# Kernel optimization log

Measured on AMD Instinct MI355X. Metric: run time of the kernel, lower is better.

The kernel has to match this reference:

```python
import jax, jax.numpy as jnp
import numpy as np

EMB = 768
HEADS = 12
HEAD_DIM = EMB // HEADS
FF = 4 * EMB
EPS = 1e-5


def setup_inputs() -> dict:
    key = jax.random.key(0)
    ks = jax.random.split(key, 12)
    s = 0.02
    return {
        "x": jax.random.normal(ks[0], (4, 2048, EMB), dtype=jnp.float32),
        "ln1_scale": jnp.ones((EMB,), jnp.float32),
        "ln1_shift": jnp.zeros((EMB,), jnp.float32),
        # weights stored [in, out] (transpose of torch Linear layout)
        "wq": jax.random.normal(ks[1], (EMB, EMB), jnp.float32) * s,
        "wk": jax.random.normal(ks[2], (EMB, EMB), jnp.float32) * s,
        "wv": jax.random.normal(ks[3], (EMB, EMB), jnp.float32) * s,
        "wo": jax.random.normal(ks[4], (EMB, EMB), jnp.float32) * s,
        "bo": jnp.zeros((EMB,), jnp.float32),
        "ln2_scale": jnp.ones((EMB,), jnp.float32),
        "ln2_shift": jnp.zeros((EMB,), jnp.float32),
        "w1": jax.random.normal(ks[5], (EMB, FF), jnp.float32) * s,
        "b1": jnp.zeros((FF,), jnp.float32),
        "w2": jax.random.normal(ks[6], (FF, EMB), jnp.float32) * s,
        "b2": jnp.zeros((EMB,), jnp.float32),
    }


def _layernorm(x, scale, shift):
    mean = jnp.mean(x, axis=-1, keepdims=True)
    var = jnp.mean(jnp.square(x - mean), axis=-1, keepdims=True)  # unbiased=False
    return scale * (x - mean) / jnp.sqrt(var + EPS) + shift


def _gelu_tanh(x):
    c = jnp.sqrt(jnp.float32(2.0 / np.pi))
    return 0.5 * x * (1.0 + jnp.tanh(c * (x + 0.044715 * x * x * x)))


def _attention(x, wq, wk, wv, wo, bo):
    b, s, _ = x.shape
    q = (x @ wq).reshape(b, s, HEADS, HEAD_DIM).transpose(0, 2, 1, 3)
    k = (x @ wk).reshape(b, s, HEADS, HEAD_DIM).transpose(0, 2, 1, 3)
    v = (x @ wv).reshape(b, s, HEADS, HEAD_DIM).transpose(0, 2, 1, 3)
    scores = jnp.einsum("bhqd,bhkd->bhqk", q, k)  # [B,H,S,S]
    causal = jnp.tril(jnp.ones((s, s), dtype=bool))
    scores = jnp.where(causal, scores, -jnp.inf)
    weights = jax.nn.softmax(scores / jnp.sqrt(jnp.float32(HEAD_DIM)), axis=-1)
    ctx = jnp.einsum("bhqk,bhkd->bhqd", weights, v)
    ctx = ctx.transpose(0, 2, 1, 3).reshape(b, s, EMB)
    return ctx @ wo + bo


def reference(x, ln1_scale, ln1_shift, wq, wk, wv, wo, bo,
              ln2_scale, ln2_shift, w1, b1, w2, b2):
    # dropout rate is 0.0 (inference) -> identity
    x = x + _attention(_layernorm(x, ln1_scale, ln1_shift), wq, wk, wv, wo, bo)
    h = _layernorm(x, ln2_scale, ln2_shift)
    h = _gelu_tanh(h @ w1 + b1) @ w2 + b2
    return x + h
```

## Files before the change

### kernel.cpp

```cpp
#include <hip/hip_runtime.h>
#include <stdint.h>

#define EMB 768
#define SEQ 2048
#define BATCH 4
#define NHEADS 12
#define HDIM 64
#define FFDIM 3072
#define NTOK (BATCH*SEQ)
#define LNEPS 1e-5f
#define QSCALE 0.1803368801111137f

typedef __attribute__((ext_vector_type(8))) short bf16x8;
typedef __attribute__((ext_vector_type(4))) float f32x4;

__device__ __forceinline__ uint16_t f2bf(float f){
  union { float f; uint32_t u; } v; v.f = f;
  uint32_t r = v.u + 0x7fffu + ((v.u >> 16) & 1u);
  return (uint16_t)(r >> 16);
}
__device__ __forceinline__ uint32_t pk_rhu(float lo, float hi){
  union { float f; uint32_t u; } a, b; a.f = lo; b.f = hi;
  return __builtin_amdgcn_perm(b.u + 0x8000u, a.u + 0x8000u, 0x07060302u);
}

typedef __attribute__((address_space(3))) uint32_t lds32_t;
typedef __attribute__((address_space(1))) const uint32_t glb32_t;
__device__ __forceinline__ void gload16(const void* g, void* l){
  __builtin_amdgcn_global_load_lds((glb32_t*)(uintptr_t)g,
                                   (lds32_t*)(uintptr_t)l, 16, 0, 0);
}

struct TPtrs { const float* src[6]; uint16_t* dst[6]; };
__global__ __launch_bounds__(256) void transpose_all(TPtrs tp){
  int idx = blockIdx.x;
  int which, bx, by, K, N;
  if (idx < 2304){ which = idx/576; int l = idx - which*576; bx = l%24; by = l/24; K = 768;  N = 768;  }
  else if (idx < 4608){ which = 4; int l = idx-2304; bx = l%96; by = l/96; K = 768;  N = 3072; }
  else { which = 5; int l = idx-4608; bx = l%24; by = l/24; K = 3072; N = 768;  }
  const float* w = tp.src[which];
  uint16_t* wt   = tp.dst[which];
  __shared__ uint16_t tile[32][33];
  int n0 = bx*32, k0 = by*32;
  #pragma unroll
  for (int i=0;i<4;i++){
    int k = threadIdx.y + i*8;
    tile[k][threadIdx.x] = f2bf(w[(size_t)(k0+k)*N + n0 + threadIdx.x]);
  }
  __syncthreads();
  #pragma unroll
  for (int i=0;i<4;i++){
    int n = threadIdx.y + i*8;
    wt[(size_t)(n0+n)*K + k0 + threadIdx.x] = tile[threadIdx.x][n];
  }
}

__global__ __launch_bounds__(256) void ln_kernel(const float* __restrict__ x,
    const float* __restrict__ sc, const float* __restrict__ sh,
    uint16_t* __restrict__ out)
{
  int row = blockIdx.x*4 + (threadIdx.x>>6);
  int ln = threadIdx.x & 63;
  const float4* xr = (const float4*)(x + (size_t)row*EMB);
  float4 v0 = xr[ln], v1 = xr[64+ln], v2 = xr[128+ln];
  float s  = v0.x+v0.y+v0.z+v0.w + v1.x+v1.y+v1.z+v1.w + v2.x+v2.y+v2.z+v2.w;
  float s2 = v0.x*v0.x+v0.y*v0.y+v0.z*v0.z+v0.w*v0.w
           + v1.x*v1.x+v1.y*v1.y+v1.z*v1.z+v1.w*v1.w
           + v2.x*v2.x+v2.y*v2.y+v2.z*v2.z+v2.w*v2.w;
  #pragma unroll
  for (int off=1;off<64;off<<=1){ s += __shfl_xor(s,off); s2 += __shfl_xor(s2,off); }
  float mean = s*(1.f/768.f);
  float var  = s2*(1.f/768.f) - mean*mean;
  float rstd = rsqrtf(var + LNEPS);
  uint16_t* orow = out + (size_t)row*EMB;
  float4 vv[3] = {v0,v1,v2};
  #pragma unroll
  for (int i=0;i<3;i++){
    int c = (i*64+ln)*4;
    ushort4 o4;
    o4.x = f2bf((vv[i].x-mean)*rstd*sc[c+0] + sh[c+0]);
    o4.y = f2bf((vv[i].y-mean)*rstd*sc[c+1] + sh[c+1]);
    o4.z = f2bf((vv[i].z-mean)*rstd*sc[c+2] + sh[c+2]);
    o4.w = f2bf((vv[i].w-mean)*rstd*sc[c+3] + sh[c+3]);
    *(ushort4*)(orow + c) = o4;
  }
}

template<int MODE, int TM>
__global__ __launch_bounds__(256, 4) void gemm_bt(const uint16_t* __restrict__ A,
    const uint16_t* __restrict__ Bt0,
    const float* __restrict__ bias,
    const float* __restrict__ resid,
    void* __restrict__ outp,
    uint16_t* __restrict__ vt_out,
    int N, int K, long bt_zstride, long out_zstride)
{
  constexpr int MI = TM/32;
  __shared__ __align__(16) uint16_t As[2][TM][32];
  __shared__ __align__(16) uint16_t Bs[2][128][32];
  const uint16_t* Bt = Bt0 + (size_t)blockIdx.z * bt_zstride;
  int tid = threadIdx.x;
  int wave = tid>>6, ln = tid&63, lane16 = ln&15, quad = ln>>4;
  int m0 = blockIdx.x*TM, n0 = blockIdx.y*128;
  int wm = (wave>>1)*(MI*16), wn = (wave&1)*64;
  f32x4 zf = {0.f,0.f,0.f,0.f};
  f32x4 acc[MI][4];
  #pragma unroll
  for (int i=0;i<MI;i++)
    #pragma unroll
    for (int j=0;j<4;j++) acc[i][j]=zf;
  int ar = tid>>2;
  int ac = (tid&3)*8;
  const uint16_t* Arow0 = A  + (size_t)(m0+ar)*K    + ac;
  const uint16_t* Arow1 = A  + (size_t)(m0+ar+64)*K + ac;
  const uint16_t* Brow0 = Bt + (size_t)(n0+ar)*K    + ac;
  const uint16_t* Brow1 = Bt + (size_t)(n0+ar+64)*K + ac;

  auto stage = [&](int buf, int k0){
    char* lA = (char*)&As[buf][0][0] + wave*1024;
    char* lB = (char*)&Bs[buf][0][0] + wave*1024;
    gload16(Arow0 + k0, lA);
    if (TM==128) gload16(Arow1 + k0, lA + 4096);
    gload16(Brow0 + k0, lB);
    gload16(Brow1 + k0, lB + 4096);
  };

  int niter = K>>5;
  stage(0, 0);
  for (int s=0; s<niter; s++){
    __syncthreads();
    if (s+1 < niter) stage((s+1)&1, (s+1)<<5);
    int buf = s&1;
    bf16x8 af[MI], bfr[4];
    #pragma unroll
    for (int mi=0;mi<MI;mi++) af[mi]  = *(const bf16x8*)&As[buf][wm+mi*16+lane16][quad*8];
    #pragma unroll
    for (int ni=0;ni<4;ni++)  bfr[ni] = *(const bf16x8*)&Bs[buf][wn+ni*16+lane16][quad*8];
    #pragma unroll
    for (int mi=0;mi<MI;mi++)
      #pragma unroll
      for (int ni=0;ni<4;ni++)
        acc[mi][ni] = __builtin_amdgcn_mfma_f32_16x16x32_bf16(af[mi], bfr[ni], acc[mi][ni], 0,0,0);
  }
  if (MODE==0 && blockIdx.z==2){
    #pragma unroll
    for (int mi=0;mi<MI;mi++){
      int mrow0 = m0 + wm + mi*16 + quad*4;
      int bb = mrow0 >> 11, s = mrow0 & 2047;
      #pragma unroll
      for (int ni=0;ni<4;ni++){
        int ncol = n0 + wn + ni*16 + lane16;
        int hh = ncol >> 6, dd = ncol & 63;
        ushort4 o4 = { f2bf(acc[mi][ni][0]), f2bf(acc[mi][ni][1]),
                       f2bf(acc[mi][ni][2]), f2bf(acc[mi][ni][3]) };
        *(ushort4*)(vt_out + ((size_t)((bb*NHEADS+hh)*HDIM + dd))*SEQ + s) = o4;
      }
    }
    return;
  }
  float oscale = (MODE==0 && blockIdx.z==0) ? QSCALE : 1.0f;
  #pragma unroll
  for (int mi=0;mi<MI;mi++){
    #pragma unroll
    for (int r=0;r<4;r++){
      int mrow = m0 + wm + mi*16 + quad*4 + r;
      #pragma unroll
      for (int ni=0;ni<4;ni++){
        int ncol = n0 + wn + ni*16 + lane16;
        float vv = acc[mi][ni][r];
        size_t idx = (size_t)mrow*N + ncol;
        if (MODE==0){
          ((uint16_t*)outp)[(size_t)blockIdx.z*out_zstride + idx] = f2bf(vv*oscale);
        } else if (MODE==1){
          ((float*)outp)[idx] = vv + bias[ncol] + resid[idx];
        } else if (MODE==2){
          float t = vv + bias[ncol];
          float u = 1.5957691216057308f*(t + 0.044715f*t*t*t);
          ((uint16_t*)outp)[idx] = f2bf(t / (1.f + __expf(-u)));
        } else {
          ((float*)outp)[idx] = vv + bias[ncol] + resid[idx];
        }
      }
    }
  }
}

__global__ __launch_bounds__(256, 3) void attn_kernel(const uint16_t* __restrict__ q,
    const uint16_t* __restrict__ k, const uint16_t* __restrict__ vt,
    uint16_t* __restrict__ ctx)
{
  __shared__ __align__(16) uint16_t Ks[2][8][64][8];
  __shared__ __align__(16) uint16_t Vs[2][8][64][8];
  const f32x4 zf = {0.f,0.f,0.f,0.f};
  int tid = threadIdx.x;
  int wave = tid>>6, ln = tid&63, l16 = ln&15, quad = ln>>4;
  int id  = blockIdx.x;
  int xcd = id & 7;
  int s_  = id >> 3;
  int p   = s_ & 15;
  int g   = xcd*6 + (s_ >> 4);
  int h   = g % NHEADS, b = g / NHEADS;
  size_t kgbase = ((size_t)(b*SEQ + ln))*EMB + h*HDIM;
  size_t vgbase = ((size_t)((b*NHEADS + h)*HDIM + ln))*SEQ;

  f32x4 o[4];
  float m_l, l_l;
  bf16x8 qf0, qf1;
  int q0w, myq;

  auto stage = [&](int buf, int kv0){
    #pragma unroll
    for (int i=0;i<2;i++){
      int c = wave + 4*i;
      gload16(k  + kgbase + (size_t)kv0*EMB + c*8, &Ks[buf][c][0][0]);
      gload16(vt + vgbase + kv0 + c*8,             &Vs[buf][c][0][0]);
    }
  };
  auto init_tile = [&](int tile){
    q0w = tile*64 + wave*16;
    myq = q0w + l16;
    const uint16_t* qrow = q + ((size_t)(b*SEQ + q0w + l16))*EMB + h*HDIM + quad*8;
    qf0 = *(const bf16x8*)(qrow);
    qf1 = *(const bf16x8*)(qrow + 32);
    o[0]=zf; o[1]=zf; o[2]=zf; o[3]=zf;
    m_l = -3.0e38f; l_l = 0.f;
  };
  auto writeout = [&](){
    float inv = 1.0f / l_l;
    uint16_t* crow = ctx + ((size_t)(b*SEQ + q0w + l16))*EMB + h*HDIM + quad*4;
    #pragma unroll
    for (int t=0; t<4; t++){
      ushort4 w4 = { f2bf(o[t][0]*inv), f2bf(o[t][1]*inv),
                     f2bf(o[t][2]*inv), f2bf(o[t][3]*inv) };
      *(ushort4*)(crow + t*16) = w4;
    }
  };
  auto compute = [&](int buf, int kv0, bool masked){
    bf16x8 kf[4][2], vf[2][4];
    #pragma unroll
    for (int f=0; f<4; f++){
      kf[f][0] = *(const bf16x8*)&Ks[buf][quad  ][f*16+l16][0];
      kf[f][1] = *(const bf16x8*)&Ks[buf][quad+4][f*16+l16][0];
    }
    #pragma unroll
    for (int t=0; t<4; t++){
      vf[0][t] = *(const bf16x8*)&Vs[buf][quad  ][t*16+l16][0];
      vf[1][t] = *(const bf16x8*)&Vs[buf][quad+4][t*16+l16][0];
    }
    f32x4 st[4];
    #pragma unroll
    for (int f=0; f<4; f++){
      st[f] = __builtin_amdgcn_mfma_f32_16x16x32_bf16(kf[f][0], qf0, zf, 0,0,0);
      st[f] = __builtin_amdgcn_mfma_f32_16x16x32_bf16(kf[f][1], qf1, st[f], 0,0,0);
    }
    if (masked){
      #pragma unroll
      for (int f=0; f<4; f++){
        int kvf = kv0 + f*16 + quad*4;
        #pragma unroll
        for (int r=0; r<4; r++)
          if (kvf + r > myq) st[f][r] = -1e30f;
      }
    }
    float cmax = -1e30f;
    #pragma unroll
    for (int f=0; f<4; f++)
      #pragma unroll
      for (int r=0; r<4; r++) cmax = fmaxf(cmax, st[f][r]);
    cmax = fmaxf(cmax, __shfl_xor(cmax,16));
    cmax = fmaxf(cmax, __shfl_xor(cmax,32));
    float mn = fmaxf(m_l, cmax);
    float alpha = __builtin_amdgcn_exp2f(m_l - mn);
    float rs = 0.f;
    #pragma unroll
    for (int f=0; f<4; f++)
      #pragma unroll
      for (int r=0; r<4; r++){
        st[f][r] = __builtin_amdgcn_exp2f(st[f][r] - mn);
        rs += st[f][r];
      }
    rs += __shfl_xor(rs,16); rs += __shfl_xor(rs,32);
    l_l = l_l*alpha + rs; m_l = mn;
    #pragma unroll
    for (int t=0; t<4; t++)
      #pragma unroll
      for (int r=0; r<4; r++) o[t][r] *= alpha;
    uint32_t dw[4][2];
    #pragma unroll
    for (int f=0; f<4; f++){
      dw[f][0] = pk_rhu(st[f][0], st[f][1]);
      dw[f][1] = pk_rhu(st[f][2], st[f][3]);
    }
    union { uint32_t u[4]; bf16x8 v; } pb[2];
    #pragma unroll
    for (int g2=0; g2<2; g2++)
      #pragma unroll
      for (int j=0; j<4; j++){
        int src = 16*(2*(quad&1) + (j>>1)) + l16;
        uint32_t lo = (uint32_t)__shfl((int)dw[2*g2  ][j&1], src, 64);
        uint32_t hi = (uint32_t)__shfl((int)dw[2*g2+1][j&1], src, 64);
        pb[g2].u[j] = (quad>>1) ? hi : lo;
      }
    #pragma unroll
    for (int t=0; t<4; t++){
      o[t] = __builtin_amdgcn_mfma_f32_16x16x32_bf16(vf[0][t], pb[0].v, o[t], 0,0,0);
      o[t] = __builtin_amdgcn_mfma_f32_16x16x32_bf16(vf[1][t], pb[1].v, o[t], 0,0,0);
    }
  };

  int n0 = p + 1, ntot = 33;
  init_tile(p);
  stage(0, 0);
  for (int s=0; s<ntot; s++){
    int sl = (s < n0) ? s : s - n0;
    int kv0 = sl*64;
    __syncthreads();
    if (s+1 < ntot){
      int sn = s+1;
      int snl = (sn < n0) ? sn : sn - n0;
      stage(sn&1, snl*64);
    }
    if (s == n0){ writeout(); init_tile(31 - p); }
    bool masked = (s == n0-1) || (s == ntot-1);
    compute(s&1, kv0, masked);
  }
  writeout();
}

extern "C" void kernel_launch(void* const* d_in, const int* in_sizes, int n_in,
                              void* d_out, int out_size, void* d_ws, size_t ws_size,
                              hipStream_t stream) {
  const float* x     = (const float*)d_in[0];
  const float* ln1_s = (const float*)d_in[1];
  const float* ln1_b = (const float*)d_in[2];
  const float* wq    = (const float*)d_in[3];
  const float* wk    = (const float*)d_in[4];
  const float* wv    = (const float*)d_in[5];
  const float* wo    = (const float*)d_in[6];
  const float* bo    = (const float*)d_in[7];
  const float* ln2_s = (const float*)d_in[8];
  const float* ln2_b = (const float*)d_in[9];
  const float* w1    = (const float*)d_in[10];
  const float* b1    = (const float*)d_in[11];
  const float* w2    = (const float*)d_in[12];
  const float* b2    = (const float*)d_in[13];

  uint16_t* wqkv_t = (uint16_t*)d_ws;
  uint16_t* wo_t   = wqkv_t + 3*EMB*EMB;
  uint16_t* w1_t   = wo_t   + EMB*EMB;
  uint16_t* w2_t   = w1_t   + (size_t)FFDIM*EMB;
  uint16_t* xn     = w2_t   + (size_t)EMB*FFDIM;
  uint16_t* qkv    = xn     + (size_t)NTOK*EMB;
  uint16_t* ctx    = qkv    + (size_t)3*NTOK*EMB;
  uint16_t* hff    = qkv;
  float*    x1     = (float*)(ctx + (size_t)NTOK*EMB);
  uint16_t* vt     = (uint16_t*)(x1 + (size_t)NTOK*EMB);

  TPtrs tp;
  tp.src[0]=wq; tp.src[1]=wk; tp.src[2]=wv; tp.src[3]=wo; tp.src[4]=w1; tp.src[5]=w2;
  tp.dst[0]=wqkv_t; tp.dst[1]=wqkv_t+EMB*EMB; tp.dst[2]=wqkv_t+2*EMB*EMB;
  tp.dst[3]=wo_t; tp.dst[4]=w1_t; tp.dst[5]=w2_t;
  transpose_all<<<6912, dim3(32,8), 0, stream>>>(tp);

  ln_kernel<<<NTOK/4, 256, 0, stream>>>(x, ln1_s, ln1_b, xn);
  gemm_bt<0,128><<<dim3(NTOK/128, EMB/128, 3), 256, 0, stream>>>(
      xn, wqkv_t, nullptr, nullptr, qkv, vt, EMB, EMB,
      (long)EMB*EMB, (long)NTOK*EMB);
  attn_kernel<<<768, 256, 0, stream>>>(
      qkv, qkv + (size_t)NTOK*EMB, vt, ctx);
  gemm_bt<1,64><<<dim3(NTOK/64, EMB/128, 1), 256, 0, stream>>>(
      ctx, wo_t, bo, x, x1, nullptr, EMB, EMB, 0, 0);
  ln_kernel<<<NTOK/4, 256, 0, stream>>>(x1, ln2_s, ln2_b, xn);
  gemm_bt<2,128><<<dim3(NTOK/128, FFDIM/128, 1), 256, 0, stream>>>(
      xn, w1_t, b1, nullptr, hff, nullptr, FFDIM, EMB, 0, 0);
  gemm_bt<3,64><<<dim3(NTOK/64, EMB/128, 1), 256, 0, stream>>>(
      hff, w2_t, b2, x1, d_out, nullptr, EMB, FFDIM, 0, 0);
}
```

Measured before the change: 380.7 us.

## Rewrite attention with 32x32 MFMA, two waves per block, lazy rescaling

The attention kernel now uses two waves per 64-query tile, with 32 queries per wave, instead of four waves with 16 each. The QK^T and PV products move from 16x16x32 to 32x32x16 bf16 MFMA, which reduces LDS fragment reloads and cross-lane shuffles when building the P operand. It also uses the hardware v_cvt_pk_bf16_f32 conversion, raises wave priority around the MFMA sections, and skips the online-softmax rescale when the running max grows by 6 or less. Each block now has fewer waves, so hiding latency depends on having more blocks resident. The skipped rescale relies on fp32 headroom to tolerate the stale max.

```diff
diff --git a/kernel.cpp b/kernel.cpp
--- a/kernel.cpp
+++ b/kernel.cpp
@@ -13,15 +13,17 @@
 
 typedef __attribute__((ext_vector_type(8))) short bf16x8;
 typedef __attribute__((ext_vector_type(4))) float f32x4;
+typedef __attribute__((ext_vector_type(16))) float f32x16;
 
 __device__ __forceinline__ uint16_t f2bf(float f){
   union { float f; uint32_t u; } v; v.f = f;
   uint32_t r = v.u + 0x7fffu + ((v.u >> 16) & 1u);
   return (uint16_t)(r >> 16);
 }
-__device__ __forceinline__ uint32_t pk_rhu(float lo, float hi){
-  union { float f; uint32_t u; } a, b; a.f = lo; b.f = hi;
-  return __builtin_amdgcn_perm(b.u + 0x8000u, a.u + 0x8000u, 0x07060302u);
+__device__ __forceinline__ uint32_t cvt_pk_bf16(float lo, float hi){
+  uint32_t d;
+  asm("v_cvt_pk_bf16_f32 %0, %1, %2" : "=v"(d) : "v"(lo), "v"(hi));
+  return d;
 }
 
 typedef __attribute__((address_space(3))) uint32_t lds32_t;
@@ -185,15 +187,14 @@
   }
 }
 
-__global__ __launch_bounds__(256, 3) void attn_kernel(const uint16_t* __restrict__ q,
+__global__ __launch_bounds__(128, 2) void attn_kernel(const uint16_t* __restrict__ q,
     const uint16_t* __restrict__ k, const uint16_t* __restrict__ vt,
     uint16_t* __restrict__ ctx)
 {
   __shared__ __align__(16) uint16_t Ks[2][8][64][8];
   __shared__ __align__(16) uint16_t Vs[2][8][64][8];
-  const f32x4 zf = {0.f,0.f,0.f,0.f};
   int tid = threadIdx.x;
-  int wave = tid>>6, ln = tid&63, l16 = ln&15, quad = ln>>4;
+  int wave = tid>>6, ln = tid&63, l32 = ln&31, h5 = ln>>5;
   int id  = blockIdx.x;
   int xcd = id & 7;
   int s_  = id >> 3;
@@ -203,109 +204,133 @@
   size_t kgbase = ((size_t)(b*SEQ + ln))*EMB + h*HDIM;
   size_t vgbase = ((size_t)((b*NHEADS + h)*HDIM + ln))*SEQ;
 
-  f32x4 o[4];
+  f32x16 o0, o1;
   float m_l, l_l;
-  bf16x8 qf0, qf1;
+  bf16x8 qb[4];
   int q0w, myq;
 
   auto stage = [&](int buf, int kv0){
     #pragma unroll
-    for (int i=0;i<2;i++){
-      int c = wave + 4*i;
+    for (int i=0;i<4;i++){
+      int c = wave + 2*i;
       gload16(k  + kgbase + (size_t)kv0*EMB + c*8, &Ks[buf][c][0][0]);
       gload16(vt + vgbase + kv0 + c*8,             &Vs[buf][c][0][0]);
     }
   };
   auto init_tile = [&](int tile){
-    q0w = tile*64 + wave*16;
-    myq = q0w + l16;
-    const uint16_t* qrow = q + ((size_t)(b*SEQ + q0w + l16))*EMB + h*HDIM + quad*8;
-    qf0 = *(const bf16x8*)(qrow);
-    qf1 = *(const bf16x8*)(qrow + 32);
-    o[0]=zf; o[1]=zf; o[2]=zf; o[3]=zf;
+    q0w = tile*64 + wave*32;
+    myq = q0w + l32;
+    const uint16_t* qrow = q + ((size_t)(b*SEQ + myq))*EMB + h*HDIM + h5*8;
+    #pragma unroll
+    for (int dm=0;dm<4;dm++) qb[dm] = *(const bf16x8*)(qrow + dm*16);
+    #pragma unroll
+    for (int r=0;r<16;r++){ o0[r]=0.f; o1[r]=0.f; }
     m_l = -3.0e38f; l_l = 0.f;
   };
   auto writeout = [&](){
     float inv = 1.0f / l_l;
-    uint16_t* crow = ctx + ((size_t)(b*SEQ + q0w + l16))*EMB + h*HDIM + quad*4;
-    #pragma unroll
-    for (int t=0; t<4; t++){
-      ushort4 w4 = { f2bf(o[t][0]*inv), f2bf(o[t][1]*inv),
-                     f2bf(o[t][2]*inv), f2bf(o[t][3]*inv) };
-      *(ushort4*)(crow + t*16) = w4;
+    uint16_t* crow = ctx + ((size_t)(b*SEQ + myq))*EMB + h*HDIM + 4*h5;
+    #pragma unroll
+    for (int rr=0; rr<4; rr++){
+      ushort4 w0 = { f2bf(o0[4*rr+0]*inv), f2bf(o0[4*rr+1]*inv),
+                     f2bf(o0[4*rr+2]*inv), f2bf(o0[4*rr+3]*inv) };
+      *(ushort4*)(crow + rr*8) = w0;
+      ushort4 w1 = { f2bf(o1[4*rr+0]*inv), f2bf(o1[4*rr+1]*inv),
+                     f2bf(o1[4*rr+2]*inv), f2bf(o1[4*rr+3]*inv) };
+      *(ushort4*)(crow + 32 + rr*8) = w1;
     }
   };
   auto compute = [&](int buf, int kv0, bool masked){
-    bf16x8 kf[4][2], vf[2][4];
-    #pragma unroll
-    for (int f=0; f<4; f++){
-      kf[f][0] = *(const bf16x8*)&Ks[buf][quad  ][f*16+l16][0];
-      kf[f][1] = *(const bf16x8*)&Ks[buf][quad+4][f*16+l16][0];
-    }
-    #pragma unroll
-    for (int t=0; t<4; t++){
-      vf[0][t] = *(const bf16x8*)&Vs[buf][quad  ][t*16+l16][0];
-      vf[1][t] = *(const bf16x8*)&Vs[buf][quad+4][t*16+l16][0];
-    }
-    f32x4 st[4];
-    #pragma unroll
-    for (int f=0; f<4; f++){
-      st[f] = __builtin_amdgcn_mfma_f32_16x16x32_bf16(kf[f][0], qf0, zf, 0,0,0);
-      st[f] = __builtin_amdgcn_mfma_f32_16x16x32_bf16(kf[f][1], qf1, st[f], 0,0,0);
-    }
+    f32x16 st0, st1;
+    #pragma unroll
+    for (int r=0;r<16;r++){ st0[r]=0.f; st1[r]=0.f; }
+    __builtin_amdgcn_s_setprio(1);
+    #pragma unroll
+    for (int dm=0;dm<4;dm++){
+      bf16x8 ka0 = *(const bf16x8*)&Ks[buf][dm*2+h5][l32][0];
+      bf16x8 ka1 = *(const bf16x8*)&Ks[buf][dm*2+h5][32+l32][0];
+      st0 = __builtin_amdgcn_mfma_f32_32x32x16_bf16(ka0, qb[dm], st0, 0,0,0);
+      st1 = __builtin_amdgcn_mfma_f32_32x32x16_bf16(ka1, qb[dm], st1, 0,0,0);
+    }
+    __builtin_amdgcn_s_setprio(0);
     if (masked){
       #pragma unroll
-      for (int f=0; f<4; f++){
-        int kvf = kv0 + f*16 + quad*4;
-        #pragma unroll
-        for (int r=0; r<4; r++)
-          if (kvf + r > myq) st[f][r] = -1e30f;
+      for (int r=0;r<16;r++){
+        int kvr = kv0 + (r&3) + 8*(r>>2) + 4*h5;
+        if (kvr      > myq) st0[r] = -1e30f;
+        if (kvr + 32 > myq) st1[r] = -1e30f;
       }
     }
-    float cmax = -1e30f;
-    #pragma unroll
-    for (int f=0; f<4; f++)
+    bf16x8 va[4][2];
+    #pragma unroll
+    for (int ks=0;ks<4;ks++){
+      va[ks][0] = *(const bf16x8*)&Vs[buf][ks*2+h5][l32][0];
+      va[ks][1] = *(const bf16x8*)&Vs[buf][ks*2+h5][32+l32][0];
+    }
+    float t[8];
+    #pragma unroll
+    for (int r=0;r<8;r++)
+      t[r] = fmaxf(fmaxf(st0[r], st0[r+8]), fmaxf(st1[r], st1[r+8]));
+    t[0]=fmaxf(t[0],t[4]); t[1]=fmaxf(t[1],t[5]);
+    t[2]=fmaxf(t[2],t[6]); t[3]=fmaxf(t[3],t[7]);
+    float cm = fmaxf(fmaxf(t[0],t[1]), fmaxf(t[2],t[3]));
+    cm = fmaxf(cm, __shfl_xor(cm, 32));
+    if (!__all(cm - m_l <= 6.0f)){
+      float mn = fmaxf(m_l, cm);
+      float alpha = __builtin_amdgcn_exp2f(m_l - mn);
+      l_l *= alpha;
       #pragma unroll
-      for (int r=0; r<4; r++) cmax = fmaxf(cmax, st[f][r]);
-    cmax = fmaxf(cmax, __shfl_xor(cmax,16));
-    cmax = fmaxf(cmax, __shfl_xor(cmax,32));
-    float mn = fmaxf(m_l, cmax);
-    float alpha = __builtin_amdgcn_exp2f(m_l - mn);
-    float rs = 0.f;
-    #pragma unroll
-    for (int f=0; f<4; f++)
-      #pragma unroll
-      for (int r=0; r<4; r++){
-        st[f][r] = __builtin_amdgcn_exp2f(st[f][r] - mn);
-        rs += st[f][r];
+      for (int r=0;r<16;r++){ o0[r]*=alpha; o1[r]*=alpha; }
+      m_l = mn;
+    }
+    #pragma unroll
+    for (int r=0;r<16;r++){
+      st0[r] = __builtin_amdgcn_exp2f(st0[r] - m_l);
+      st1[r] = __builtin_amdgcn_exp2f(st1[r] - m_l);
+    }
+    float s0=0.f, s1=0.f, s2=0.f, s3=0.f;
+    #pragma unroll
+    for (int r=0;r<16;r+=4){
+      s0 += st0[r+0] + st1[r+0];
+      s1 += st0[r+1] + st1[r+1];
+      s2 += st0[r+2] + st1[r+2];
+      s3 += st0[r+3] + st1[r+3];
+    }
+    float rs = (s0+s1)+(s2+s3);
+    rs += __shfl_xor(rs, 32);
+    l_l += rs;
+    bf16x8 pbv[4];
+    #pragma unroll
+    for (int ks=0;ks<4;ks++){
+      const int bs = (ks&1)*8;
+      uint32_t c0,c1,c2,c3;
+      if (ks < 2){
+        c0 = cvt_pk_bf16(st0[bs+0], st0[bs+1]);
+        c1 = cvt_pk_bf16(st0[bs+2], st0[bs+3]);
+        c2 = cvt_pk_bf16(st0[bs+4], st0[bs+5]);
+        c3 = cvt_pk_bf16(st0[bs+6], st0[bs+7]);
+      } else {
+        c0 = cvt_pk_bf16(st1[bs+0], st1[bs+1]);
+        c1 = cvt_pk_bf16(st1[bs+2], st1[bs+3]);
+        c2 = cvt_pk_bf16(st1[bs+4], st1[bs+5]);
+        c3 = cvt_pk_bf16(st1[bs+6], st1[bs+7]);
       }
-    rs += __shfl_xor(rs,16); rs += __shfl_xor(rs,32);
-    l_l = l_l*alpha + rs; m_l = mn;
-    #pragma unroll
-    for (int t=0; t<4; t++)
-      #pragma unroll
-      for (int r=0; r<4; r++) o[t][r] *= alpha;
-    uint32_t dw[4][2];
-    #pragma unroll
-    for (int f=0; f<4; f++){
-      dw[f][0] = pk_rhu(st[f][0], st[f][1]);
-      dw[f][1] = pk_rhu(st[f][2], st[f][3]);
-    }
-    union { uint32_t u[4]; bf16x8 v; } pb[2];
-    #pragma unroll
-    for (int g2=0; g2<2; g2++)
-      #pragma unroll
-      for (int j=0; j<4; j++){
-        int src = 16*(2*(quad&1) + (j>>1)) + l16;
-        uint32_t lo = (uint32_t)__shfl((int)dw[2*g2  ][j&1], src, 64);
-        uint32_t hi = (uint32_t)__shfl((int)dw[2*g2+1][j&1], src, 64);
-        pb[g2].u[j] = (quad>>1) ? hi : lo;
-      }
-    #pragma unroll
-    for (int t=0; t<4; t++){
-      o[t] = __builtin_amdgcn_mfma_f32_16x16x32_bf16(vf[0][t], pb[0].v, o[t], 0,0,0);
-      o[t] = __builtin_amdgcn_mfma_f32_16x16x32_bf16(vf[1][t], pb[1].v, o[t], 0,0,0);
-    }
+      uint32_t ya = (uint32_t)__shfl_xor((int)(h5 ? c0 : c2), 32);
+      uint32_t yb = (uint32_t)__shfl_xor((int)(h5 ? c1 : c3), 32);
+      union { uint32_t u[4]; bf16x8 v; } pu;
+      pu.u[0] = h5 ? ya : c0;
+      pu.u[1] = h5 ? yb : c1;
+      pu.u[2] = h5 ? c2 : ya;
+      pu.u[3] = h5 ? c3 : yb;
+      pbv[ks] = pu.v;
+    }
+    __builtin_amdgcn_s_setprio(1);
+    #pragma unroll
+    for (int ks=0;ks<4;ks++){
+      o0 = __builtin_amdgcn_mfma_f32_32x32x16_bf16(va[ks][0], pbv[ks], o0, 0,0,0);
+      o1 = __builtin_amdgcn_mfma_f32_32x32x16_bf16(va[ks][1], pbv[ks], o1, 0,0,0);
+    }
+    __builtin_amdgcn_s_setprio(0);
   };
 
   int n0 = p + 1, ntot = 33;
@@ -366,7 +391,7 @@
   gemm_bt<0,128><<<dim3(NTOK/128, EMB/128, 3), 256, 0, stream>>>(
       xn, wqkv_t, nullptr, nullptr, qkv, vt, EMB, EMB,
       (long)EMB*EMB, (long)NTOK*EMB);
-  attn_kernel<<<768, 256, 0, stream>>>(
+  attn_kernel<<<768, 128, 0, stream>>>(
       qkv, qkv + (size_t)NTOK*EMB, vt, ctx);
   gemm_bt<1,64><<<dim3(NTOK/64, EMB/128, 1), 256, 0, stream>>>(
       ctx, wo_t, bo, x, x1, nullptr, EMB, EMB, 0, 0);
```

New measurement: 391.4 us. 1.03x slower.
